# Kernel optimization log

Hardware: AMD Instinct MI355X
Metric: run time of the kernel (lower is better)

The kernel has to match this reference:

```python
import jax, jax.numpy as jnp
import numpy as np

MARGIN = 0.3
NEG_FILL = -100.0
EPS = 1e-6


def setup_inputs() -> dict:
    key = jax.random.key(0)
    k1, k2, k3 = jax.random.split(key, 3)
    B, N, D = 256, 131072, 128
    xembs = jax.random.normal(k1, (B, D), dtype=jnp.float32)
    yembs = jax.random.normal(k2, (N, D), dtype=jnp.float32)
    pos_inds = jax.random.randint(k3, (B, 1), 0, N, dtype=jnp.int64)
    # target: multi-hot label matrix; positives marked 1 at pos_inds
    target = jnp.zeros((B, N), dtype=jnp.float32)
    target = target.at[jnp.arange(B)[:, None], pos_inds].set(1.0)
    return {"xembs": xembs, "yembs": yembs, "target": target,
            "pos_inds": pos_inds, "num_neg": 5}


def reference(xembs, yembs, target, pos_inds, num_neg):
    # sim: [B, N]
    sim = xembs @ yembs.T
    # positive similarities: [B, 1]
    sim_p = jnp.take_along_axis(sim, pos_inds, axis=1)
    # mask out positives, mine hardest negatives
    neg_sim = jnp.where(target < EPS, sim, NEG_FILL)
    _, idx = jax.lax.top_k(neg_sim, num_neg)          # [B, num_neg]
    sim_n = jnp.take_along_axis(sim, idx, axis=1)      # [B, num_neg]
    # hinge triplet loss
    loss = jnp.maximum(jnp.zeros_like(sim_n), sim_n - sim_p + MARGIN)
    mask = (loss != 0).astype(loss.dtype)
    prob = jax.nn.softmax(sim_n * mask, axis=1)
    return (loss * prob).mean()
```

## Files before the change

### kernel.cpp

```cpp
#include <hip/hip_runtime.h>

#define BROWS 256
#define NCOLS 131072
#define DDIM  128
#define K     5
#define MARGIN 0.3f

#define NBLK  512
#define CPB   (NCOLS / NBLK)
#define NIT   (CPB / 16)
#define ZGATE 3.4f
#define CAP   128
#define YSTR  68

typedef __attribute__((ext_vector_type(8))) __bf16 bf16x8;
typedef __attribute__((ext_vector_type(4))) float f32x4;
typedef __attribute__((ext_vector_type(4))) unsigned int u32x4;

__device__ __forceinline__ unsigned pack_bf16(float a, float b) {
    unsigned ua = __float_as_uint(a), ub = __float_as_uint(b);
    unsigned ra = (ua + 0x7fffu + ((ua >> 16) & 1u)) >> 16;
    unsigned rb = (ub + 0x7fffu + ((ub >> 16) & 1u)) & 0xffff0000u;
    return ra | rb;
}

__device__ __forceinline__ u32x4 pack8(const float4& a, const float4& b) {
    u32x4 t;
    t[0] = pack_bf16(a.x, a.y); t[1] = pack_bf16(a.z, a.w);
    t[2] = pack_bf16(b.x, b.y); t[3] = pack_bf16(b.z, b.w);
    return t;
}

__global__ __launch_bounds__(256) void init_kernel(
    const float* __restrict__ x, float* __restrict__ thr,
    int* __restrict__ cnt, float* __restrict__ out)
{
    const int t = threadIdx.x;
    const float* xp = x + (size_t)t * DDIM;
    float s = 0.f;
#pragma unroll
    for (int k = 0; k < DDIM; k += 4) {
        const float4 v = *(const float4*)(xp + k);
        s = fmaf(v.x, v.x, s); s = fmaf(v.y, v.y, s);
        s = fmaf(v.z, v.z, s); s = fmaf(v.w, v.w, s);
    }
    thr[t] = ZGATE * sqrtf(s);
    cnt[t] = 0;
    if (t == 0) out[0] = 0.f;
}

__global__ __launch_bounds__(256, 2) void gemm_collect_kernel(
    const float* __restrict__ x, const float* __restrict__ y,
    const float* __restrict__ thr,
    int* __restrict__ cnt, float* __restrict__ bufv, int* __restrict__ bufc)
{
    __shared__ unsigned ybf[2][16 * YSTR];

    const int tid   = threadIdx.x;
    const int lane  = tid & 63;
    const int quad  = lane >> 4;
    const int l15   = lane & 15;
    const int wrow0 = tid & 192;
    const int col0  = blockIdx.x * CPB;

    bf16x8 af[4][4];
#pragma unroll
    for (int mt = 0; mt < 4; ++mt) {
        const float* xp = x + (size_t)(wrow0 + mt * 16 + l15) * DDIM + quad * 8;
#pragma unroll
        for (int s = 0; s < 4; ++s) {
            const float4 a = *(const float4*)(xp + s * 32);
            const float4 b = *(const float4*)(xp + s * 32 + 4);
            const u32x4 t = pack8(a, b);
            af[mt][s] = __builtin_bit_cast(bf16x8, t);
        }
    }

    float thrv[16];
#pragma unroll
    for (int mt = 0; mt < 4; ++mt)
#pragma unroll
        for (int r = 0; r < 4; ++r)
            thrv[mt * 4 + r] = thr[wrow0 + mt * 16 + quad * 4 + r];

    const int sc = tid >> 4, sj = tid & 15;
    const float* ysrc = y + (size_t)(col0 + sc) * DDIM + sj * 8;
    const unsigned sdst = sc * YSTR + sj * 4;
    const unsigned frag_off = l15 * YSTR + quad * 4;

    float4 ga = *(const float4*)(ysrc);
    float4 gb = *(const float4*)(ysrc + 4);
    *(u32x4*)(&ybf[0][0] + sdst) = pack8(ga, gb);

    for (int it = 0; it < NIT; ++it) {
        if (it + 1 < NIT) {
            const float* yn = ysrc + (size_t)(it + 1) * 16 * DDIM;
            ga = *(const float4*)(yn);
            gb = *(const float4*)(yn + 4);
        }
        __syncthreads();

        const unsigned* yb = &ybf[it & 1][0];
        bf16x8 bfrag[4];
#pragma unroll
        for (int s = 0; s < 4; ++s)
            bfrag[s] = __builtin_bit_cast(bf16x8, *(const u32x4*)(yb + frag_off + s * 16));

        f32x4 acc[4];
#pragma unroll
        for (int mt = 0; mt < 4; ++mt) acc[mt] = (f32x4){0.f, 0.f, 0.f, 0.f};
#pragma unroll
        for (int s = 0; s < 4; ++s)
#pragma unroll
            for (int mt = 0; mt < 4; ++mt)
                acc[mt] = __builtin_amdgcn_mfma_f32_16x16x32_bf16(af[mt][s], bfrag[s], acc[mt], 0, 0, 0);

        if (it + 1 < NIT)
            *(u32x4*)(&ybf[(it + 1) & 1][0] + sdst) = pack8(ga, gb);

        float m = -1.f;
#pragma unroll
        for (int mt = 0; mt < 4; ++mt)
#pragma unroll
            for (int r = 0; r < 4; ++r)
                m = fmaxf(m, acc[mt][r] - thrv[mt * 4 + r]);
        if (m > 0.f) {
            const int col = col0 + it * 16 + l15;
#pragma unroll
            for (int mt = 0; mt < 4; ++mt)
#pragma unroll
                for (int r = 0; r < 4; ++r) {
                    const float v = acc[mt][r];
                    if (v > thrv[mt * 4 + r]) {
                        const int row = wrow0 + mt * 16 + quad * 4 + r;
                        const int idx = atomicAdd(&cnt[row], 1);
                        if (idx < CAP) {
                            bufv[row * CAP + idx] = v;
                            bufc[row * CAP + idx] = col;
                        }
                    }
                }
        }
    }
}

__device__ __forceinline__ void insert5(float* t5, float v) {
    if (v > t5[K - 1]) {
        float nv = v;
#pragma unroll
        for (int p = 0; p < K; ++p) {
            const bool gt = nv > t5[p];
            const float tv = t5[p];
            if (gt) { t5[p] = nv; nv = tv; }
        }
    }
}

__device__ __forceinline__ void merge5(float* __restrict__ t5, const float* __restrict__ src) {
#pragma unroll
    for (int p = 0; p < K; ++p) insert5(t5, src[p]);
}

__device__ __forceinline__ float epilogue(const float* t5, float sp) {
    float loss[K], logit[K];
#pragma unroll
    for (int p = 0; p < K; ++p) {
        loss[p]  = fmaxf(0.f, t5[p] - sp + MARGIN);
        logit[p] = (loss[p] != 0.f) ? t5[p] : 0.f;
    }
    float mx = logit[0];
#pragma unroll
    for (int p = 1; p < K; ++p) mx = fmaxf(mx, logit[p]);
    float den = 0.f, num = 0.f;
#pragma unroll
    for (int p = 0; p < K; ++p) {
        const float e = __expf(logit[p] - mx);
        den += e;
        num += loss[p] * e;
    }
    return num / den;
}

__global__ __launch_bounds__(256) void reduce_kernel(
    const float* __restrict__ x, const float* __restrict__ y,
    const int* __restrict__ pos, const int* __restrict__ cnt,
    const float* __restrict__ bufv, const int* __restrict__ bufc,
    int* __restrict__ flag, float* __restrict__ out)
{
    const int row = blockIdx.x;
    const int tid = threadIdx.x;
    __shared__ float sred[256];
    __shared__ float sv[256 * K];

    const int prow = pos[row];
    float p = 0.f;
    if (tid < DDIM) p = x[row * DDIM + tid] * y[(size_t)prow * DDIM + tid];
    sred[tid] = p;
    __syncthreads();
    for (int s = 128; s >= 1; s >>= 1) {
        if (tid < s) sred[tid] += sred[tid + s];
        __syncthreads();
    }

    const int c = cnt[row];
    const int n = c < CAP ? c : CAP;
    float t5[K];
#pragma unroll
    for (int q = 0; q < K; ++q) t5[q] = -3.0e38f;
    if (tid < n && bufc[row * CAP + tid] != prow)
        t5[0] = bufv[row * CAP + tid];

#pragma unroll
    for (int q = 0; q < K; ++q) sv[tid * K + q] = t5[q];
    __syncthreads();
    for (int s = 128; s >= 1; s >>= 1) {
        if (tid < s) {
            merge5(t5, &sv[(tid + s) * K]);
#pragma unroll
            for (int q = 0; q < K; ++q) sv[tid * K + q] = t5[q];
        }
        __syncthreads();
    }

    if (tid == 0) {
        const bool ok = (c <= CAP) && (t5[K - 1] > -1.0e38f);
        flag[row] = ok ? 0 : 1;
        if (ok) atomicAdd(out, epilogue(t5, sred[0]) * (1.0f / (BROWS * K)));
    }
}

__global__ __launch_bounds__(256) void fallback_kernel(
    const float* __restrict__ x, const float* __restrict__ y,
    const int* __restrict__ pos, const int* __restrict__ flag,
    float* __restrict__ out)
{
    const int row = blockIdx.x;
    if (flag[row] == 0) return;
    const int tid = threadIdx.x;
    const int prow = pos[row];
    __shared__ float xr[DDIM];
    __shared__ float sv[256 * K];
    if (tid < DDIM) xr[tid] = x[row * DDIM + tid];
    __syncthreads();

    float t5[K];
#pragma unroll
    for (int q = 0; q < K; ++q) t5[q] = -3.0e38f;
    for (int col = tid; col < NCOLS; col += 256) {
        if (col == prow) continue;
        const float* yp = y + (size_t)col * DDIM;
        float d = 0.f;
        for (int k = 0; k < DDIM; ++k) d = fmaf(xr[k], yp[k], d);
        insert5(t5, d);
    }
#pragma unroll
    for (int q = 0; q < K; ++q) sv[tid * K + q] = t5[q];
    __syncthreads();
    for (int s = 128; s >= 1; s >>= 1) {
        if (tid < s) {
            merge5(t5, &sv[(tid + s) * K]);
#pragma unroll
            for (int q = 0; q < K; ++q) sv[tid * K + q] = t5[q];
        }
        __syncthreads();
    }
    if (tid == 0) {
        float sp = 0.f;
        const float* yp = y + (size_t)prow * DDIM;
        for (int k = 0; k < DDIM; ++k) sp = fmaf(xr[k], yp[k], sp);
        atomicAdd(out, epilogue(t5, sp) * (1.0f / (BROWS * K)));
    }
}

extern "C" void kernel_launch(void* const* d_in, const int* in_sizes, int n_in,
                              void* d_out, int out_size, void* d_ws, size_t ws_size,
                              hipStream_t stream) {
    const float* x  = (const float*)d_in[0];
    const float* y  = (const float*)d_in[1];
    const int* pos  = (const int*)d_in[3];

    int*   cnt  = (int*)d_ws;
    int*   flag = cnt + BROWS;
    float* thr  = (float*)(flag + BROWS);
    float* bufv = thr + BROWS;
    int*   bufc = (int*)(bufv + (size_t)BROWS * CAP);

    init_kernel<<<dim3(1), 256, 0, stream>>>(x, thr, cnt, (float*)d_out);
    gemm_collect_kernel<<<dim3(NBLK), 256, 0, stream>>>(x, y, thr, cnt, bufv, bufc);
    reduce_kernel<<<dim3(BROWS), 256, 0, stream>>>(x, y, pos, cnt, bufv, bufc, flag, (float*)d_out);
    fallback_kernel<<<dim3(BROWS), 256, 0, stream>>>(x, y, pos, flag, (float*)d_out);
}
```

Baseline: 237.2 us.

## Fuse init into GEMM, use per-block candidate regions with LDS counters

Removes the separate init kernel by computing row-norm thresholds inside the GEMM kernel using warp shuffles, and zeroes the output from block 0. Candidate collection now goes through a shared-memory counter into per-block region buffers of packed (value, row|col) entries, replacing global per-row atomics. The reduce kernel scans every region and filters by row. The change also adds a two-deep register prefetch of y tiles and uses a hardware bf16 pack builtin when available. The reduce kernel now has every row block scan all 512 regions, which adds redundant reads. The out zeroing in block 0 is not ordered against other launches' atomics, but the later kernels run after it, so that is fine.

```diff
diff --git a/kernel.cpp b/kernel.cpp
--- a/kernel.cpp
+++ b/kernel.cpp
@@ -10,7 +10,7 @@
 #define CPB   (NCOLS / NBLK)
 #define NIT   (CPB / 16)
 #define ZGATE 3.4f
-#define CAP   128
+#define RCAP  96
 #define YSTR  68
 
 typedef __attribute__((ext_vector_type(8))) __bf16 bf16x8;
@@ -18,10 +18,15 @@
 typedef __attribute__((ext_vector_type(4))) unsigned int u32x4;
 
 __device__ __forceinline__ unsigned pack_bf16(float a, float b) {
+#if defined(__has_builtin) && __has_builtin(__builtin_amdgcn_cvt_pk_bf16_f32)
+    auto r = __builtin_amdgcn_cvt_pk_bf16_f32(a, b);
+    return __builtin_bit_cast(unsigned, r);
+#else
     unsigned ua = __float_as_uint(a), ub = __float_as_uint(b);
     unsigned ra = (ua + 0x7fffu + ((ua >> 16) & 1u)) >> 16;
     unsigned rb = (ub + 0x7fffu + ((ub >> 16) & 1u)) & 0xffff0000u;
     return ra | rb;
+#endif
 }
 
 __device__ __forceinline__ u32x4 pack8(const float4& a, const float4& b) {
@@ -31,30 +36,12 @@
     return t;
 }
 
-__global__ __launch_bounds__(256) void init_kernel(
-    const float* __restrict__ x, float* __restrict__ thr,
-    int* __restrict__ cnt, float* __restrict__ out)
-{
-    const int t = threadIdx.x;
-    const float* xp = x + (size_t)t * DDIM;
-    float s = 0.f;
-#pragma unroll
-    for (int k = 0; k < DDIM; k += 4) {
-        const float4 v = *(const float4*)(xp + k);
-        s = fmaf(v.x, v.x, s); s = fmaf(v.y, v.y, s);
-        s = fmaf(v.z, v.z, s); s = fmaf(v.w, v.w, s);
-    }
-    thr[t] = ZGATE * sqrtf(s);
-    cnt[t] = 0;
-    if (t == 0) out[0] = 0.f;
-}
-
 __global__ __launch_bounds__(256, 2) void gemm_collect_kernel(
     const float* __restrict__ x, const float* __restrict__ y,
-    const float* __restrict__ thr,
-    int* __restrict__ cnt, float* __restrict__ bufv, int* __restrict__ bufc)
+    uint2* __restrict__ regions, int* __restrict__ nbs, float* __restrict__ outz)
 {
     __shared__ unsigned ybf[2][16 * YSTR];
+    __shared__ int lcnt;
 
     const int tid   = threadIdx.x;
     const int lane  = tid & 63;
@@ -63,40 +50,60 @@
     const int wrow0 = tid & 192;
     const int col0  = blockIdx.x * CPB;
 
+    if (blockIdx.x == 0 && tid == 0) outz[0] = 0.f;
+    if (tid == 0) lcnt = 0;
+
     bf16x8 af[4][4];
+    float nrm[4];
 #pragma unroll
     for (int mt = 0; mt < 4; ++mt) {
         const float* xp = x + (size_t)(wrow0 + mt * 16 + l15) * DDIM + quad * 8;
+        float s2 = 0.f;
 #pragma unroll
         for (int s = 0; s < 4; ++s) {
             const float4 a = *(const float4*)(xp + s * 32);
             const float4 b = *(const float4*)(xp + s * 32 + 4);
+            s2 = fmaf(a.x, a.x, s2); s2 = fmaf(a.y, a.y, s2);
+            s2 = fmaf(a.z, a.z, s2); s2 = fmaf(a.w, a.w, s2);
+            s2 = fmaf(b.x, b.x, s2); s2 = fmaf(b.y, b.y, s2);
+            s2 = fmaf(b.z, b.z, s2); s2 = fmaf(b.w, b.w, s2);
             const u32x4 t = pack8(a, b);
             af[mt][s] = __builtin_bit_cast(bf16x8, t);
         }
-    }
-
+        nrm[mt] = s2;
+    }
+    float myThr[4];
+#pragma unroll
+    for (int mt = 0; mt < 4; ++mt) {
+        float s2 = nrm[mt];
+        s2 += __shfl_xor(s2, 16);
+        s2 += __shfl_xor(s2, 32);
+        myThr[mt] = ZGATE * sqrtf(s2);
+    }
     float thrv[16];
 #pragma unroll
     for (int mt = 0; mt < 4; ++mt)
 #pragma unroll
         for (int r = 0; r < 4; ++r)
-            thrv[mt * 4 + r] = thr[wrow0 + mt * 16 + quad * 4 + r];
+            thrv[mt * 4 + r] = __shfl(myThr[mt], quad * 4 + r);
 
     const int sc = tid >> 4, sj = tid & 15;
     const float* ysrc = y + (size_t)(col0 + sc) * DDIM + sj * 8;
     const unsigned sdst = sc * YSTR + sj * 4;
     const unsigned frag_off = l15 * YSTR + quad * 4;
 
-    float4 ga = *(const float4*)(ysrc);
-    float4 gb = *(const float4*)(ysrc + 4);
-    *(u32x4*)(&ybf[0][0] + sdst) = pack8(ga, gb);
+    float4 ga[2], gb[2];
+    ga[0] = *(const float4*)(ysrc);
+    gb[0] = *(const float4*)(ysrc + 4);
+    ga[1] = *(const float4*)(ysrc + 16 * DDIM);
+    gb[1] = *(const float4*)(ysrc + 16 * DDIM + 4);
+    *(u32x4*)(&ybf[0][0] + sdst) = pack8(ga[0], gb[0]);
 
     for (int it = 0; it < NIT; ++it) {
-        if (it + 1 < NIT) {
-            const float* yn = ysrc + (size_t)(it + 1) * 16 * DDIM;
-            ga = *(const float4*)(yn);
-            gb = *(const float4*)(yn + 4);
+        if (it + 2 < NIT) {
+            const float* yn = ysrc + (size_t)(it + 2) * 16 * DDIM;
+            ga[it & 1] = *(const float4*)(yn);
+            gb[it & 1] = *(const float4*)(yn + 4);
         }
         __syncthreads();
 
@@ -116,7 +123,7 @@
                 acc[mt] = __builtin_amdgcn_mfma_f32_16x16x32_bf16(af[mt][s], bfrag[s], acc[mt], 0, 0, 0);
 
         if (it + 1 < NIT)
-            *(u32x4*)(&ybf[(it + 1) & 1][0] + sdst) = pack8(ga, gb);
+            *(u32x4*)(&ybf[(it + 1) & 1][0] + sdst) = pack8(ga[(it + 1) & 1], gb[(it + 1) & 1]);
 
         float m = -1.f;
 #pragma unroll
@@ -132,16 +139,19 @@
                 for (int r = 0; r < 4; ++r) {
                     const float v = acc[mt][r];
                     if (v > thrv[mt * 4 + r]) {
-                        const int row = wrow0 + mt * 16 + quad * 4 + r;
-                        const int idx = atomicAdd(&cnt[row], 1);
-                        if (idx < CAP) {
-                            bufv[row * CAP + idx] = v;
-                            bufc[row * CAP + idx] = col;
+                        const int idx = atomicAdd(&lcnt, 1);
+                        if (idx < RCAP) {
+                            const int row = wrow0 + mt * 16 + quad * 4 + r;
+                            regions[blockIdx.x * RCAP + idx] =
+                                make_uint2(__float_as_uint(v), ((unsigned)row << 17) | (unsigned)col);
                         }
                     }
                 }
         }
     }
+
+    __syncthreads();
+    if (tid == 0) nbs[blockIdx.x] = lcnt;
 }
 
 __device__ __forceinline__ void insert5(float* t5, float v) {
@@ -183,14 +193,16 @@
 
 __global__ __launch_bounds__(256) void reduce_kernel(
     const float* __restrict__ x, const float* __restrict__ y,
-    const int* __restrict__ pos, const int* __restrict__ cnt,
-    const float* __restrict__ bufv, const int* __restrict__ bufc,
+    const int* __restrict__ pos,
+    const uint2* __restrict__ regions, const int* __restrict__ nbs,
     int* __restrict__ flag, float* __restrict__ out)
 {
     const int row = blockIdx.x;
     const int tid = threadIdx.x;
     __shared__ float sred[256];
     __shared__ float sv[256 * K];
+    __shared__ int sover;
+    if (tid == 0) sover = 0;
 
     const int prow = pos[row];
     float p = 0.f;
@@ -202,13 +214,21 @@
         __syncthreads();
     }
 
-    const int c = cnt[row];
-    const int n = c < CAP ? c : CAP;
     float t5[K];
 #pragma unroll
     for (int q = 0; q < K; ++q) t5[q] = -3.0e38f;
-    if (tid < n && bufc[row * CAP + tid] != prow)
-        t5[0] = bufv[row * CAP + tid];
+    int over = 0;
+    for (int reg = tid; reg < NBLK; reg += 256) {
+        int nb = nbs[reg];
+        if (nb > RCAP) { over = 1; nb = RCAP; }
+        const uint2* rp = regions + (size_t)reg * RCAP;
+        for (int i = 0; i < nb; ++i) {
+            const uint2 e = rp[i];
+            const int r = (int)(e.y >> 17), c = (int)(e.y & 0x1FFFFu);
+            if (r == row && c != prow) insert5(t5, __uint_as_float(e.x));
+        }
+    }
+    if (over) sover = 1;
 
 #pragma unroll
     for (int q = 0; q < K; ++q) sv[tid * K + q] = t5[q];
@@ -223,7 +243,7 @@
     }
 
     if (tid == 0) {
-        const bool ok = (c <= CAP) && (t5[K - 1] > -1.0e38f);
+        const bool ok = (sover == 0) && (t5[K - 1] > -1.0e38f);
         flag[row] = ok ? 0 : 1;
         if (ok) atomicAdd(out, epilogue(t5, sred[0]) * (1.0f / (BROWS * K)));
     }
@@ -279,14 +299,11 @@
     const float* y  = (const float*)d_in[1];
     const int* pos  = (const int*)d_in[3];
 
-    int*   cnt  = (int*)d_ws;
-    int*   flag = cnt + BROWS;
-    float* thr  = (float*)(flag + BROWS);
-    float* bufv = thr + BROWS;
-    int*   bufc = (int*)(bufv + (size_t)BROWS * CAP);
-
-    init_kernel<<<dim3(1), 256, 0, stream>>>(x, thr, cnt, (float*)d_out);
-    gemm_collect_kernel<<<dim3(NBLK), 256, 0, stream>>>(x, y, thr, cnt, bufv, bufc);
-    reduce_kernel<<<dim3(BROWS), 256, 0, stream>>>(x, y, pos, cnt, bufv, bufc, flag, (float*)d_out);
+    uint2* regions = (uint2*)d_ws;
+    int*   nbs     = (int*)(regions + (size_t)NBLK * RCAP);
+    int*   flag    = nbs + NBLK;
+
+    gemm_collect_kernel<<<dim3(NBLK), 256, 0, stream>>>(x, y, regions, nbs, (float*)d_out);
+    reduce_kernel<<<dim3(BROWS), 256, 0, stream>>>(x, y, pos, regions, nbs, flag, (float*)d_out);
     fallback_kernel<<<dim3(BROWS), 256, 0, stream>>>(x, y, pos, flag, (float*)d_out);
 }
```

Result: slower. 269.9 us (+13.8%).
